# Optimization experiments

Measured on AMD Instinct MI355X. Metric: run time of the kernel, lower is better.

## Reference

```python
import jax, jax.numpy as jnp
import numpy as np

B, N_CAM, D_BINS, HF, WF, C = 1, 6, 118, 32, 88, 80
DZ, DY, DX = 1, 128, 128
N_POINTS = 1_000_000
BEV_FEAT_SHAPE = (B, DZ, DY, DX, C)  # (B, Dz, Dy, Dx, C)


def setup_inputs() -> dict:
    key = jax.random.key(0)
    k1, k2, k3, k4, k5 = jax.random.split(key, 5)
    depth = jax.random.uniform(k1, (B, N_CAM, D_BINS, HF, WF), dtype=jnp.float32)
    feat = jax.random.normal(k2, (B, N_CAM, HF, WF, C), dtype=jnp.float32)
    n_depth = B * N_CAM * D_BINS * HF * WF      # flattened depth size
    n_feat_rows = B * N_CAM * HF * WF           # rows of flattened feat
    n_bev = B * DZ * DY * DX                    # flattened BEV grid size
    ranks_depths = jax.random.randint(k3, (N_POINTS,), 0, n_depth, dtype=jnp.int32)
    ranks_feats = jax.random.randint(k4, (N_POINTS,), 0, n_feat_rows, dtype=jnp.int32)
    ranks_bevs = jnp.sort(jax.random.randint(k5, (N_POINTS,), 0, n_bev, dtype=jnp.int32))
    # intervals consistent with sorted ranks_bevs (contiguous runs of equal bev rank)
    rb = np.asarray(ranks_bevs)
    change = np.concatenate([[True], rb[1:] != rb[:-1]])
    starts = np.flatnonzero(change)
    lengths = np.diff(np.append(starts, len(rb)))
    return {
        "depth": depth,
        "feat": feat,
        "ranks_depths": ranks_depths,
        "ranks_feats": ranks_feats,
        "ranks_bevs": ranks_bevs,
        "bev_feat_shape": BEV_FEAT_SHAPE,
        "interval_starts": jnp.asarray(starts, dtype=jnp.int32),
        "interval_lengths": jnp.asarray(lengths, dtype=jnp.int32),
    }


def reference(depth, feat, ranks_depths, ranks_feats, ranks_bevs,
              bev_feat_shape, interval_starts, interval_lengths):
    # bev_pool_v2: gather depth scalar and feat row per point, multiply,
    # scatter-sum into the BEV grid. Interval-based summation over sorted
    # ranks_bevs is mathematically a segment-sum keyed by ranks_bevs, so we
    # use segment_sum directly (intervals are redundant metadata).
    b, dz, dy, dx, c = bev_feat_shape
    d = depth.reshape(-1)[ranks_depths]               # [P]
    f = feat.reshape(-1, c)[ranks_feats]              # [P, C]
    out = jax.ops.segment_sum(f * d[:, None], ranks_bevs,
                              num_segments=b * dz * dy * dx)  # [B*Dz*Dy*Dx, C]
    out = out.reshape(b, dz, dy, dx, c)
    return jnp.transpose(out, (0, 4, 1, 2, 3))        # (B, C, Dz, Dy, Dx)
```

## Files before the change

### kernel.cpp

```cpp
#include <hip/hip_runtime.h>
#include <hip/hip_bf16.h>


#define C_CH 80
#define CPT  20

__global__ void bev_pool_f4_kernel(
    const float*  __restrict__ depth,
    const float4* __restrict__ feat4,
    const int*    __restrict__ ranks_depth,
    const int*    __restrict__ ranks_feat,
    const int*    __restrict__ ranks_bev,
    const int*    __restrict__ interval_starts,
    const int*    __restrict__ interval_lengths,
    int n_intervals,
    int n_bev,
    float* __restrict__ out)
{
    int idx = blockIdx.x * blockDim.x + threadIdx.x;
    int total = n_intervals * CPT;
    if (idx >= total) return;

    int interval = idx / CPT;
    int c4       = idx - interval * CPT;

    int start = interval_starts[interval];
    int len   = interval_lengths[interval];

    float4 acc = make_float4(0.f, 0.f, 0.f, 0.f);

    int len4 = len & ~3;
    int i = 0;
    for (; i < len4; i += 4) {
        int p0 = start + i, p1 = p0 + 1, p2 = p0 + 2, p3 = p0 + 3;
        int rd0 = ranks_depth[p0], rd1 = ranks_depth[p1];
        int rd2 = ranks_depth[p2], rd3 = ranks_depth[p3];
        int rf0 = ranks_feat[p0],  rf1 = ranks_feat[p1];
        int rf2 = ranks_feat[p2],  rf3 = ranks_feat[p3];
        float d0 = depth[rd0], d1 = depth[rd1], d2 = depth[rd2], d3 = depth[rd3];
        float4 f0 = feat4[(long)rf0 * CPT + c4];
        float4 f1 = feat4[(long)rf1 * CPT + c4];
        float4 f2 = feat4[(long)rf2 * CPT + c4];
        float4 f3 = feat4[(long)rf3 * CPT + c4];
        acc.x += d0 * f0.x; acc.y += d0 * f0.y; acc.z += d0 * f0.z; acc.w += d0 * f0.w;
        acc.x += d1 * f1.x; acc.y += d1 * f1.y; acc.z += d1 * f1.z; acc.w += d1 * f1.w;
        acc.x += d2 * f2.x; acc.y += d2 * f2.y; acc.z += d2 * f2.z; acc.w += d2 * f2.w;
        acc.x += d3 * f3.x; acc.y += d3 * f3.y; acc.z += d3 * f3.z; acc.w += d3 * f3.w;
    }
    for (; i < len; ++i) {
        int pp = start + i;
        float d = depth[ranks_depth[pp]];
        float4 f = feat4[(long)ranks_feat[pp] * CPT + c4];
        acc.x += d * f.x; acc.y += d * f.y; acc.z += d * f.z; acc.w += d * f.w;
    }

    int bev = ranks_bev[start];
    long o = (long)(c4 * 4) * n_bev + bev;
    out[o]             = acc.x;
    out[o + n_bev]     = acc.y;
    out[o + 2 * n_bev] = acc.z;
    out[o + 3 * n_bev] = acc.w;
}

extern "C" void kernel_launch(void* const* d_in, const int* in_sizes, int n_in,
                              void* d_out, int out_size, void* d_ws, size_t ws_size,
                              hipStream_t stream) {
    const float* depth = (const float*)d_in[0];
    const float4* feat4 = (const float4*)d_in[1];
    const int* ranks_depth = (const int*)d_in[2];
    const int* ranks_feat  = (const int*)d_in[3];
    const int* ranks_bev   = (const int*)d_in[4];
    const int* interval_starts  = (const int*)d_in[6];
    const int* interval_lengths = (const int*)d_in[7];

    int n_intervals = in_sizes[6];
    int n_bev = out_size / C_CH;
    float* out = (float*)d_out;

    hipMemsetAsync(d_out, 0, (size_t)out_size * sizeof(float), stream);

    int total = n_intervals * CPT;
    int block = 256;
    int grid = (total + block - 1) / block;
    bev_pool_f4_kernel<<<grid, block, 0, stream>>>(
        depth, feat4, ranks_depth, ranks_feat, ranks_bev,
        interval_starts, interval_lengths, n_intervals, n_bev, out);
}
```

Baseline: 136.0 us.

## Split points into fixed chunks with atomic flushes instead of per-interval threads

Replaces the one-thread-per-interval-per-channel-group scheme with fixed 16-point chunks that walk the sorted bev ranks, flushing partial sums via atomicAdd whenever the bev rank changes. It also loads the rank arrays as int4 vectors. The aim is more threads and even per-thread work to hide gather latency, and it no longer uses the interval metadata. In exchange it adds many float atomics at chunk and run boundaries, and summation order is no longer deterministic.

After: 364.0 us. 168% more time.

```diff
diff --git a/kernel.cpp b/kernel.cpp
--- a/kernel.cpp
+++ b/kernel.cpp
@@ -2,87 +2,91 @@
 #include <hip/hip_bf16.h>
 
 
-#define C_CH 80
-#define CPT  20
+#define C_CH  80
+#define CPT   20
+#define CHUNK 16
 
-__global__ void bev_pool_f4_kernel(
+__global__ void bev_pool_chunk_kernel(
     const float*  __restrict__ depth,
     const float4* __restrict__ feat4,
-    const int*    __restrict__ ranks_depth,
-    const int*    __restrict__ ranks_feat,
-    const int*    __restrict__ ranks_bev,
-    const int*    __restrict__ interval_starts,
-    const int*    __restrict__ interval_lengths,
-    int n_intervals,
+    const int*    __restrict__ rd,
+    const int*    __restrict__ rf,
+    const int*    __restrict__ rb,
+    int P,
     int n_bev,
     float* __restrict__ out)
 {
     int idx = blockIdx.x * blockDim.x + threadIdx.x;
-    int total = n_intervals * CPT;
-    if (idx >= total) return;
+    int n_chunks = (P + CHUNK - 1) / CHUNK;
+    if (idx >= n_chunks * CPT) return;
 
-    int interval = idx / CPT;
-    int c4       = idx - interval * CPT;
-
-    int start = interval_starts[interval];
-    int len   = interval_lengths[interval];
+    int chunk = idx / CPT;
+    int c4    = idx - chunk * CPT;
+    int p0    = chunk * CHUNK;
+    int pend  = min(p0 + CHUNK, P);
 
     float4 acc = make_float4(0.f, 0.f, 0.f, 0.f);
+    int cur = rb[p0];
+    long obase = (long)(c4 * 4) * n_bev;
 
-    int len4 = len & ~3;
-    int i = 0;
-    for (; i < len4; i += 4) {
-        int p0 = start + i, p1 = p0 + 1, p2 = p0 + 2, p3 = p0 + 3;
-        int rd0 = ranks_depth[p0], rd1 = ranks_depth[p1];
-        int rd2 = ranks_depth[p2], rd3 = ranks_depth[p3];
-        int rf0 = ranks_feat[p0],  rf1 = ranks_feat[p1];
-        int rf2 = ranks_feat[p2],  rf3 = ranks_feat[p3];
-        float d0 = depth[rd0], d1 = depth[rd1], d2 = depth[rd2], d3 = depth[rd3];
-        float4 f0 = feat4[(long)rf0 * CPT + c4];
-        float4 f1 = feat4[(long)rf1 * CPT + c4];
-        float4 f2 = feat4[(long)rf2 * CPT + c4];
-        float4 f3 = feat4[(long)rf3 * CPT + c4];
+#define FLUSH(BEV) do { \
+        atomicAdd(out + obase + (BEV), acc.x); \
+        atomicAdd(out + obase + (long)n_bev + (BEV), acc.y); \
+        atomicAdd(out + obase + 2L * n_bev + (BEV), acc.z); \
+        atomicAdd(out + obase + 3L * n_bev + (BEV), acc.w); \
+        acc = make_float4(0.f, 0.f, 0.f, 0.f); \
+    } while (0)
+
+    int p = p0;
+    for (; p + 4 <= pend; p += 4) {
+        int4 rd4 = *reinterpret_cast<const int4*>(rd + p);
+        int4 rf4 = *reinterpret_cast<const int4*>(rf + p);
+        int4 rb4 = *reinterpret_cast<const int4*>(rb + p);
+        float  d0 = depth[rd4.x], d1 = depth[rd4.y], d2 = depth[rd4.z], d3 = depth[rd4.w];
+        float4 f0 = feat4[(long)rf4.x * CPT + c4];
+        float4 f1 = feat4[(long)rf4.y * CPT + c4];
+        float4 f2 = feat4[(long)rf4.z * CPT + c4];
+        float4 f3 = feat4[(long)rf4.w * CPT + c4];
+
+        if (rb4.x != cur) { FLUSH(cur); cur = rb4.x; }
         acc.x += d0 * f0.x; acc.y += d0 * f0.y; acc.z += d0 * f0.z; acc.w += d0 * f0.w;
+        if (rb4.y != cur) { FLUSH(cur); cur = rb4.y; }
         acc.x += d1 * f1.x; acc.y += d1 * f1.y; acc.z += d1 * f1.z; acc.w += d1 * f1.w;
+        if (rb4.z != cur) { FLUSH(cur); cur = rb4.z; }
         acc.x += d2 * f2.x; acc.y += d2 * f2.y; acc.z += d2 * f2.z; acc.w += d2 * f2.w;
+        if (rb4.w != cur) { FLUSH(cur); cur = rb4.w; }
         acc.x += d3 * f3.x; acc.y += d3 * f3.y; acc.z += d3 * f3.z; acc.w += d3 * f3.w;
     }
-    for (; i < len; ++i) {
-        int pp = start + i;
-        float d = depth[ranks_depth[pp]];
-        float4 f = feat4[(long)ranks_feat[pp] * CPT + c4];
+    for (; p < pend; ++p) {
+        int b = rb[p];
+        float  d = depth[rd[p]];
+        float4 f = feat4[(long)rf[p] * CPT + c4];
+        if (b != cur) { FLUSH(cur); cur = b; }
         acc.x += d * f.x; acc.y += d * f.y; acc.z += d * f.z; acc.w += d * f.w;
     }
-
-    int bev = ranks_bev[start];
-    long o = (long)(c4 * 4) * n_bev + bev;
-    out[o]             = acc.x;
-    out[o + n_bev]     = acc.y;
-    out[o + 2 * n_bev] = acc.z;
-    out[o + 3 * n_bev] = acc.w;
+    FLUSH(cur);
+#undef FLUSH
 }
 
 extern "C" void kernel_launch(void* const* d_in, const int* in_sizes, int n_in,
                               void* d_out, int out_size, void* d_ws, size_t ws_size,
                               hipStream_t stream) {
-    const float* depth = (const float*)d_in[0];
+    const float*  depth = (const float*)d_in[0];
     const float4* feat4 = (const float4*)d_in[1];
     const int* ranks_depth = (const int*)d_in[2];
     const int* ranks_feat  = (const int*)d_in[3];
     const int* ranks_bev   = (const int*)d_in[4];
-    const int* interval_starts  = (const int*)d_in[6];
-    const int* interval_lengths = (const int*)d_in[7];
 
-    int n_intervals = in_sizes[6];
+    int P = in_sizes[2];
     int n_bev = out_size / C_CH;
     float* out = (float*)d_out;
 
     hipMemsetAsync(d_out, 0, (size_t)out_size * sizeof(float), stream);
 
-    int total = n_intervals * CPT;
+    int n_chunks = (P + CHUNK - 1) / CHUNK;
+    int total = n_chunks * CPT;
     int block = 256;
     int grid = (total + block - 1) / block;
-    bev_pool_f4_kernel<<<grid, block, 0, stream>>>(
-        depth, feat4, ranks_depth, ranks_feat, ranks_bev,
-        interval_starts, interval_lengths, n_intervals, n_bev, out);
+    bev_pool_chunk_kernel<<<grid, block, 0, stream>>>(
+        depth, feat4, ranks_depth, ranks_feat, ranks_bev, P, n_bev, out);
 }
```

## Split each BEV interval's points across threads with shared-memory reduction

Applied to the files above, without the earlier changes.

Instead of one thread walking every point of an interval for its float4 channel slice, each interval's points are strided over 8 split threads. Per-split partial sums are combined through shared memory and written by split 0. Each block handles 2 intervals at 320 threads. This is meant to shorten the long serial chains of dependent gathers and expose more memory-level parallelism. The cost is a block-level sync, shared-memory traffic and more threads doing redundant index loads.

Result: no change. 134.9 us (-0.8%).

```diff
diff --git a/kernel.cpp b/kernel.cpp
--- a/kernel.cpp
+++ b/kernel.cpp
@@ -2,70 +2,88 @@
 #include <hip/hip_bf16.h>
 
 
-#define C_CH 80
-#define CPT  20
+#define C_CH   80
+#define QPT    20
+#define SPLITS 8
+#define IPB    2
+#define BLOCK  (IPB * QPT * SPLITS)
 
-__global__ void bev_pool_f4_kernel(
+__global__ __launch_bounds__(BLOCK) void bev_pool_split_kernel(
     const float*  __restrict__ depth,
     const float4* __restrict__ feat4,
-    const int*    __restrict__ ranks_depth,
-    const int*    __restrict__ ranks_feat,
-    const int*    __restrict__ ranks_bev,
-    const int*    __restrict__ interval_starts,
-    const int*    __restrict__ interval_lengths,
+    const int*    __restrict__ rd,
+    const int*    __restrict__ rf,
+    const int*    __restrict__ rb,
+    const int*    __restrict__ istart,
+    const int*    __restrict__ ilen,
     int n_intervals,
     int n_bev,
     float* __restrict__ out)
 {
-    int idx = blockIdx.x * blockDim.x + threadIdx.x;
-    int total = n_intervals * CPT;
-    if (idx >= total) return;
+    __shared__ float4 red[IPB][SPLITS][QPT];
 
-    int interval = idx / CPT;
-    int c4       = idx - interval * CPT;
-
-    int start = interval_starts[interval];
-    int len   = interval_lengths[interval];
+    int tid   = threadIdx.x;
+    int il    = tid / (QPT * SPLITS);
+    int r     = tid - il * (QPT * SPLITS);
+    int split = r / QPT;
+    int quad  = r - split * QPT;
+    int interval = blockIdx.x * IPB + il;
+    bool valid = interval < n_intervals;
 
     float4 acc = make_float4(0.f, 0.f, 0.f, 0.f);
+    int start = 0, len = 0, bev = 0;
 
-    int len4 = len & ~3;
-    int i = 0;
-    for (; i < len4; i += 4) {
-        int p0 = start + i, p1 = p0 + 1, p2 = p0 + 2, p3 = p0 + 3;
-        int rd0 = ranks_depth[p0], rd1 = ranks_depth[p1];
-        int rd2 = ranks_depth[p2], rd3 = ranks_depth[p3];
-        int rf0 = ranks_feat[p0],  rf1 = ranks_feat[p1];
-        int rf2 = ranks_feat[p2],  rf3 = ranks_feat[p3];
-        float d0 = depth[rd0], d1 = depth[rd1], d2 = depth[rd2], d3 = depth[rd3];
-        float4 f0 = feat4[(long)rf0 * CPT + c4];
-        float4 f1 = feat4[(long)rf1 * CPT + c4];
-        float4 f2 = feat4[(long)rf2 * CPT + c4];
-        float4 f3 = feat4[(long)rf3 * CPT + c4];
-        acc.x += d0 * f0.x; acc.y += d0 * f0.y; acc.z += d0 * f0.z; acc.w += d0 * f0.w;
-        acc.x += d1 * f1.x; acc.y += d1 * f1.y; acc.z += d1 * f1.z; acc.w += d1 * f1.w;
-        acc.x += d2 * f2.x; acc.y += d2 * f2.y; acc.z += d2 * f2.z; acc.w += d2 * f2.w;
-        acc.x += d3 * f3.x; acc.y += d3 * f3.y; acc.z += d3 * f3.z; acc.w += d3 * f3.w;
-    }
-    for (; i < len; ++i) {
-        int pp = start + i;
-        float d = depth[ranks_depth[pp]];
-        float4 f = feat4[(long)ranks_feat[pp] * CPT + c4];
-        acc.x += d * f.x; acc.y += d * f.y; acc.z += d * f.z; acc.w += d * f.w;
+    if (valid) {
+        start = istart[interval];
+        len   = ilen[interval];
+        bev   = rb[start];
+
+        int i = split;
+        for (; i + SPLITS < len; i += 2 * SPLITS) {
+            int p0 = start + i;
+            int p1 = p0 + SPLITS;
+            int rd0 = rd[p0], rf0 = rf[p0];
+            int rd1 = rd[p1], rf1 = rf[p1];
+            float d0 = depth[rd0];
+            float d1 = depth[rd1];
+            float4 f0 = feat4[(long)rf0 * QPT + quad];
+            float4 f1 = feat4[(long)rf1 * QPT + quad];
+            acc.x += d0 * f0.x; acc.y += d0 * f0.y;
+            acc.z += d0 * f0.z; acc.w += d0 * f0.w;
+            acc.x += d1 * f1.x; acc.y += d1 * f1.y;
+            acc.z += d1 * f1.z; acc.w += d1 * f1.w;
+        }
+        if (i < len) {
+            int p = start + i;
+            float d = depth[rd[p]];
+            float4 f = feat4[(long)rf[p] * QPT + quad];
+            acc.x += d * f.x; acc.y += d * f.y;
+            acc.z += d * f.z; acc.w += d * f.w;
+        }
     }
 
-    int bev = ranks_bev[start];
-    long o = (long)(c4 * 4) * n_bev + bev;
-    out[o]             = acc.x;
-    out[o + n_bev]     = acc.y;
-    out[o + 2 * n_bev] = acc.z;
-    out[o + 3 * n_bev] = acc.w;
+    red[il][split][quad] = acc;
+    __syncthreads();
+
+    if (valid && split == 0) {
+        float4 s = acc;
+        #pragma unroll
+        for (int k = 1; k < SPLITS; ++k) {
+            float4 t = red[il][k][quad];
+            s.x += t.x; s.y += t.y; s.z += t.z; s.w += t.w;
+        }
+        long o = (long)(quad * 4) * n_bev + bev;
+        out[o]             = s.x;
+        out[o + n_bev]     = s.y;
+        out[o + 2L * n_bev] = s.z;
+        out[o + 3L * n_bev] = s.w;
+    }
 }
 
 extern "C" void kernel_launch(void* const* d_in, const int* in_sizes, int n_in,
                               void* d_out, int out_size, void* d_ws, size_t ws_size,
                               hipStream_t stream) {
-    const float* depth = (const float*)d_in[0];
+    const float*  depth = (const float*)d_in[0];
     const float4* feat4 = (const float4*)d_in[1];
     const int* ranks_depth = (const int*)d_in[2];
     const int* ranks_feat  = (const int*)d_in[3];
@@ -79,10 +97,8 @@
 
     hipMemsetAsync(d_out, 0, (size_t)out_size * sizeof(float), stream);
 
-    int total = n_intervals * CPT;
-    int block = 256;
-    int grid = (total + block - 1) / block;
-    bev_pool_f4_kernel<<<grid, block, 0, stream>>>(
+    int grid = (n_intervals + IPB - 1) / IPB;
+    bev_pool_split_kernel<<<grid, BLOCK, 0, stream>>>(
         depth, feat4, ranks_depth, ranks_feat, ranks_bev,
         interval_starts, interval_lengths, n_intervals, n_bev, out);
 }
```
